# Performance work log

Hardware: AMD Instinct MI355X
Metric: run time of the kernel (lower is better)

Reference implementation:

```python
import jax, jax.numpy as jnp
import numpy as np

HEAD_NUM = 16
EMBED_DIM = 1024
HIDDEN_DIM = 1024
HEAD_DIM = HIDDEN_DIM // HEAD_NUM


def setup_inputs() -> dict:
    key = jax.random.key(0)
    ks = jax.random.split(key, 7)
    B, S = 2, 2048
    X = jax.random.normal(ks[0], (B, S, EMBED_DIM), dtype=jnp.float32)
    sc = 1.0 / np.sqrt(EMBED_DIM)
    Wq = jax.random.normal(ks[1], (EMBED_DIM, HIDDEN_DIM), dtype=jnp.float32) * sc
    Wk = jax.random.normal(ks[2], (EMBED_DIM, HIDDEN_DIM), dtype=jnp.float32) * sc
    Wv = jax.random.normal(ks[3], (EMBED_DIM, HIDDEN_DIM), dtype=jnp.float32) * sc
    bq = jax.random.normal(ks[4], (HIDDEN_DIM,), dtype=jnp.float32) * 0.01
    bk = jax.random.normal(ks[5], (HIDDEN_DIM,), dtype=jnp.float32) * 0.01
    bv = jax.random.normal(ks[6], (HIDDEN_DIM,), dtype=jnp.float32) * 0.01
    return {"X": X, "Wq": Wq, "bq": bq, "Wk": Wk, "bk": bk, "Wv": Wv, "bv": bv}


def reference(X, Wq, bq, Wk, bk, Wv, bv):
    B, S, _ = X.shape
    # projections -> [B, H, S, D]
    def split_heads(t):
        return t.reshape(B, S, HEAD_NUM, HEAD_DIM).transpose(0, 2, 1, 3)
    Q = split_heads(X @ Wq + bq)
    K = split_heads(X @ Wk + bk)  # computed but unused, faithful to source bug
    V = split_heads(X @ Wv + bv)
    # NOTE: source computes Q @ V^T (bug), reproduced faithfully
    scores = jnp.einsum('bhqd,bhkd->bhqk', Q, V) / np.sqrt(HEAD_DIM)
    attn = jax.nn.softmax(scores, axis=-1)  # dropout is identity in eval
    out = jnp.einsum('bhqk,bhkd->bhqd', attn, V)
    return out.transpose(0, 2, 1, 3).reshape(B, S, HIDDEN_DIM)
```

## Files before the change

### kernel.cpp

```cpp
#include <hip/hip_runtime.h>
#include <math.h>


constexpr int BATCH = 2;
constexpr int SEQ   = 2048;
constexpr int EMB   = 1024;
constexpr int NHEAD = 16;
constexpr int HDIM  = 64;
constexpr int HID   = 1024;

typedef __attribute__((ext_vector_type(8))) _Float16 half8;
typedef __attribute__((ext_vector_type(4))) float    f32x4;

#define MFMA16(a, b, c) __builtin_amdgcn_mfma_f32_16x16x32_f16((a), (b), (c), 0, 0, 0)

constexpr int LDT = 80;

#define QK_SCALE 0.18033688011112042f
#define LOG2_THR 11.0f

__device__ __forceinline__ _Float16 f2h(float f) { return (_Float16)f; }

__global__ __launch_bounds__(256) void conv_wt_kernel(
    const float* __restrict__ W0, _Float16* __restrict__ WT0,
    const float* __restrict__ W1, _Float16* __restrict__ WT1)
{
    const float*  W  = blockIdx.z ? W1  : W0;
    _Float16*     WT = blockIdx.z ? WT1 : WT0;
    __shared__ _Float16 T[64 * 68];
    const int tid = threadIdx.x;
    const int n0 = blockIdx.x * 64;
    const int k0 = blockIdx.y * 64;

    #pragma unroll
    for (int i = 0; i < 4; ++i) {
        const int u = tid + i * 256;
        const int r = u >> 4;
        const int c4 = (u & 15) << 2;
        const float4 v = *(const float4*)&W[(size_t)(k0 + r) * HID + n0 + c4];
        T[r * 68 + c4 + 0] = f2h(v.x);
        T[r * 68 + c4 + 1] = f2h(v.y);
        T[r * 68 + c4 + 2] = f2h(v.z);
        T[r * 68 + c4 + 3] = f2h(v.w);
    }
    __syncthreads();

    union Pack { uint4 q; _Float16 e[8]; };
    #pragma unroll
    for (int i = 0; i < 2; ++i) {
        const int u = tid + i * 256;
        const int n = u >> 3;
        const int kc = (u & 7) << 3;
        Pack p;
        #pragma unroll
        for (int j = 0; j < 8; ++j) p.e[j] = T[(kc + j) * 68 + n];
        *(uint4*)&WT[(size_t)(n0 + n) * EMB + k0 + kc] = p.q;
    }
}

__global__ __launch_bounds__(256) void proj_kernel(
    const float* __restrict__ X, const _Float16* __restrict__ WTq,
    const _Float16* __restrict__ WTv, const float* __restrict__ bq,
    const float* __restrict__ bv, _Float16* __restrict__ Qo,
    _Float16* __restrict__ Vo, _Float16* __restrict__ VTo)
{
    __shared__ __align__(16) _Float16 Xs[64 * LDT];
    __shared__ __align__(16) _Float16 Wqs[64 * LDT];
    __shared__ __align__(16) _Float16 Wvs[64 * LDT];

    const int tid  = threadIdx.x;
    const int lane = tid & 63;
    const int w    = tid >> 6;
    const int l15  = lane & 15;
    const int l4   = lane >> 4;
    const int wg   = blockIdx.x;
    const int nid  = (wg & 7) * 128 + (wg >> 3);
    const int mblk = nid >> 4;
    const int h    = nid & 15;
    const int m0   = mblk * 64;
    const int n0   = h * HDIM;

    f32x4 aq[4], av[4];
    #pragma unroll
    for (int nt = 0; nt < 4; ++nt) {
        aq[nt] = f32x4{0.f, 0.f, 0.f, 0.f};
        av[nt] = f32x4{0.f, 0.f, 0.f, 0.f};
    }

    for (int k0 = 0; k0 < EMB; k0 += 64) {
        #pragma unroll
        for (int i = 0; i < 4; ++i) {
            const int u = tid + i * 256;
            const int r = u >> 4;
            const int c4 = (u & 15) << 2;
            const float4 v = *(const float4*)&X[(size_t)(m0 + r) * EMB + k0 + c4];
            Xs[r * LDT + c4 + 0] = f2h(v.x);
            Xs[r * LDT + c4 + 1] = f2h(v.y);
            Xs[r * LDT + c4 + 2] = f2h(v.z);
            Xs[r * LDT + c4 + 3] = f2h(v.w);
        }
        #pragma unroll
        for (int i = 0; i < 2; ++i) {
            const int u = tid + i * 256;
            const int r = u >> 3;
            const int c8 = (u & 7) << 3;
            *(uint4*)&Wqs[r * LDT + c8] =
                *(const uint4*)&WTq[(size_t)(n0 + r) * EMB + k0 + c8];
            *(uint4*)&Wvs[r * LDT + c8] =
                *(const uint4*)&WTv[(size_t)(n0 + r) * EMB + k0 + c8];
        }
        __syncthreads();

        __builtin_amdgcn_s_setprio(1);
        #pragma unroll
        for (int kd = 0; kd < 2; ++kd) {
            const int ko = kd * 32 + l4 * 8;
            half8 xa = *(const half8*)&Xs[(w * 16 + l15) * LDT + ko];
            #pragma unroll
            for (int nt = 0; nt < 4; ++nt) {
                half8 wq = *(const half8*)&Wqs[(nt * 16 + l15) * LDT + ko];
                half8 wv = *(const half8*)&Wvs[(nt * 16 + l15) * LDT + ko];
                aq[nt] = MFMA16(xa, wq, aq[nt]);
                av[nt] = MFMA16(xa, wv, av[nt]);
            }
        }
        __builtin_amdgcn_s_setprio(0);
        __syncthreads();
    }

    constexpr int LV = 65;
    _Float16* Vlds = Xs;
    const int bb = m0 >> 11;
    const int sb = m0 & (SEQ - 1);
    const int bh = bb * NHEAD + h;

    #pragma unroll
    for (int nt = 0; nt < 4; ++nt) {
        const int d = nt * 16 + l15;
        const float bqv = bq[n0 + d];
        const float bvv = bv[n0 + d];
        #pragma unroll
        for (int r = 0; r < 4; ++r) {
            const int sl = w * 16 + l4 * 4 + r;
            const int s  = sb + sl;
            const _Float16 vh = f2h(av[nt][r] + bvv);
            Qo[((size_t)bh * SEQ + s) * HDIM + d] =
                f2h((aq[nt][r] + bqv) * QK_SCALE);
            Vo[((size_t)bh * SEQ + s) * HDIM + d] = vh;
            Vlds[sl * LV + d] = vh;
        }
    }
    __syncthreads();

    union PK { uint4 q; _Float16 e[8]; };
    #pragma unroll
    for (int i = 0; i < 2; ++i) {
        const int c  = tid + i * 256;
        const int d  = c >> 3;
        const int sc = (c & 7) << 3;
        PK p;
        #pragma unroll
        for (int j = 0; j < 8; ++j) p.e[j] = Vlds[(sc + j) * LV + d];
        *(uint4*)&VTo[((size_t)bh * HDIM + d) * SEQ + sb + sc] = p.q;
    }
}

__global__ __launch_bounds__(256) void attn_kernel(
    const _Float16* __restrict__ Qw, const _Float16* __restrict__ Vw,
    const _Float16* __restrict__ VTw, float* __restrict__ out)
{
    __shared__ __align__(16) _Float16 PQs[64 * LDT];
    __shared__ __align__(16) _Float16 Vs[64 * LDT];
    __shared__ __align__(16) _Float16 VTs[80 * LDT];

    const int tid  = threadIdx.x;
    const int lane = tid & 63;
    const int w    = tid >> 6;
    const int l15  = lane & 15;
    const int l4   = lane >> 4;
    const int wg = blockIdx.x;
    const int nw = (wg & 7) * 128 + (wg >> 3);
    const int bh = nw >> 5;
    const int qb = nw & 31;
    const int b  = bh >> 4;
    const int h  = bh & (NHEAD - 1);
    const int s0 = qb * 64;

    const _Float16* Qp  = Qw  + (size_t)bh * SEQ * HDIM;
    const _Float16* Vp  = Vw  + (size_t)bh * SEQ * HDIM;
    const _Float16* VTp = VTw + (size_t)bh * HDIM * SEQ;

    auto stageV = [&](int t) {
        const int u0 = tid,       r0 = u0 >> 3, c0 = (u0 & 7) << 3;
        const int u1 = tid + 256, r1 = u1 >> 3, c1 = (u1 & 7) << 3;
        uint4 a0 = *(const uint4*)&Vp [(size_t)(t * 64 + r0) * HDIM + c0];
        uint4 a1 = *(const uint4*)&Vp [(size_t)(t * 64 + r1) * HDIM + c1];
        uint4 b0 = *(const uint4*)&VTp[(size_t)r0 * SEQ + t * 64 + c0];
        uint4 b1 = *(const uint4*)&VTp[(size_t)r1 * SEQ + t * 64 + c1];
        *(uint4*)&Vs [r0 * LDT + c0] = a0;
        *(uint4*)&Vs [r1 * LDT + c1] = a1;
        *(uint4*)&VTs[r0 * LDT + c0] = b0;
        *(uint4*)&VTs[r1 * LDT + c1] = b1;
    };

    #pragma unroll
    for (int i = 0; i < 2; ++i) {
        const int u = tid + i * 256, r = u >> 3, c8 = (u & 7) << 3;
        *(uint4*)&PQs[r * LDT + c8] =
            *(const uint4*)&Qp[(size_t)(s0 + r) * HDIM + c8];
    }
    #pragma unroll
    for (int i = 0; i < 5; ++i) {
        const int idx = tid + i * 256;
        if (idx < 16 * LDT)
            VTs[64 * LDT + idx] = (idx < LDT) ? (_Float16)1.0f : (_Float16)0.0f;
    }
    stageV(0);
    __syncthreads();

    const half8 qa0 = *(const half8*)&PQs[(w * 16 + l15) * LDT + l4 * 8];
    const half8 qa1 = *(const half8*)&PQs[(w * 16 + l15) * LDT + 32 + l4 * 8];

    f32x4 acc_o[5];
    #pragma unroll
    for (int dt = 0; dt < 5; ++dt) acc_o[dt] = f32x4{0.f, 0.f, 0.f, 0.f};
    float m_i[4] = {-INFINITY, -INFINITY, -INFINITY, -INFINITY};

    const int chi  = l15 >> 3;
    const int hl   = l15 & 7;
    const int rkey = l15 & 7;

    for (int t = 0; t < SEQ / 64; ++t) {
        f32x4 acc_s[4];
        #pragma unroll
        for (int nt = 0; nt < 4; ++nt) acc_s[nt] = f32x4{0.f, 0.f, 0.f, 0.f};
        __builtin_amdgcn_s_setprio(1);
        #pragma unroll
        for (int nt = 0; nt < 4; ++nt) {
            half8 vb0 = *(const half8*)&Vs[(nt * 16 + l15) * LDT + l4 * 8];
            half8 vb1 = *(const half8*)&Vs[(nt * 16 + l15) * LDT + 32 + l4 * 8];
            acc_s[nt] = MFMA16(qa0, vb0, acc_s[nt]);
            acc_s[nt] = MFMA16(qa1, vb1, acc_s[nt]);
        }
        __builtin_amdgcn_s_setprio(0);

        float mloc[4];
        int needf = 0;
        #pragma unroll
        for (int r = 0; r < 4; ++r) {
            float ml = fmaxf(fmaxf(acc_s[0][r], acc_s[1][r]),
                             fmaxf(acc_s[2][r], acc_s[3][r]));
            #pragma unroll
            for (int off = 1; off < 16; off <<= 1)
                ml = fmaxf(ml, __shfl_xor(ml, off));
            mloc[r] = ml;
            needf |= (ml > m_i[r] + LOG2_THR) ? 1 : 0;
        }
        if (__any(needf)) {
            #pragma unroll
            for (int r = 0; r < 4; ++r) {
                const float mnew = fmaxf(m_i[r], mloc[r]);
                const float corr = __builtin_amdgcn_exp2f(m_i[r] - mnew);
                m_i[r] = mnew;
                #pragma unroll
                for (int dt = 0; dt < 5; ++dt) acc_o[dt][r] *= corr;
            }
        }
        #pragma unroll
        for (int r = 0; r < 4; ++r) {
            const float p0 = __builtin_amdgcn_exp2f(acc_s[0][r] - m_i[r]);
            const float p1 = __builtin_amdgcn_exp2f(acc_s[1][r] - m_i[r]);
            const float p2 = __builtin_amdgcn_exp2f(acc_s[2][r] - m_i[r]);
            const float p3 = __builtin_amdgcn_exp2f(acc_s[3][r] - m_i[r]);
            const int key = (l4 * 4 + r) & 7;
            _Float16* pr = &PQs[(w * 16 + l4 * 4 + r) * LDT];
            pr[(((0 + chi) ^ key) << 3) + hl] = f2h(p0);
            pr[(((2 + chi) ^ key) << 3) + hl] = f2h(p1);
            pr[(((4 + chi) ^ key) << 3) + hl] = f2h(p2);
            pr[(((6 + chi) ^ key) << 3) + hl] = f2h(p3);
        }

        const _Float16* prd = &PQs[(w * 16 + l15) * LDT];
        half8 pa0 = *(const half8*)&prd[((l4 ^ rkey) << 3)];
        half8 pa1 = *(const half8*)&prd[(((4 + l4) ^ rkey) << 3)];
        __builtin_amdgcn_s_setprio(1);
        #pragma unroll
        for (int dt = 0; dt < 5; ++dt) {
            half8 vt0 = *(const half8*)&VTs[(dt * 16 + l15) * LDT + l4 * 8];
            half8 vt1 = *(const half8*)&VTs[(dt * 16 + l15) * LDT + 32 + l4 * 8];
            acc_o[dt] = MFMA16(pa0, vt0, acc_o[dt]);
            acc_o[dt] = MFMA16(pa1, vt1, acc_o[dt]);
        }
        __builtin_amdgcn_s_setprio(0);

        __syncthreads();
        if (t + 1 < SEQ / 64) {
            stageV(t + 1);
            __syncthreads();
        }
    }

    #pragma unroll
    for (int r = 0; r < 4; ++r) {
        const float ls  = __shfl(acc_o[4][r], (lane & 48));
        const float inv = 1.f / ls;
        const int s = s0 + w * 16 + l4 * 4 + r;
        float* op = &out[((size_t)(b * SEQ + s)) * HID + h * HDIM + l15];
        op[ 0] = acc_o[0][r] * inv;
        op[16] = acc_o[1][r] * inv;
        op[32] = acc_o[2][r] * inv;
        op[48] = acc_o[3][r] * inv;
    }
}

extern "C" void kernel_launch(void* const* d_in, const int* in_sizes, int n_in,
                              void* d_out, int out_size, void* d_ws, size_t ws_size,
                              hipStream_t stream) {
    (void)in_sizes; (void)n_in; (void)out_size; (void)ws_size;
    const float* X  = (const float*)d_in[0];
    const float* Wq = (const float*)d_in[1];
    const float* bq = (const float*)d_in[2];
    const float* Wv = (const float*)d_in[5];
    const float* bv = (const float*)d_in[6];
    float* outp = (float*)d_out;

    char* ws = (char*)d_ws;
    _Float16* WTq = (_Float16*)(ws);
    _Float16* WTv = (_Float16*)(ws + (2u  << 20));
    _Float16* Qb  = (_Float16*)(ws + (4u  << 20));
    _Float16* Vb  = (_Float16*)(ws + (12u << 20));
    _Float16* VTb = (_Float16*)(ws + (20u << 20));

    conv_wt_kernel<<<dim3(16, 16, 2), 256, 0, stream>>>(Wq, WTq, Wv, WTv);
    proj_kernel<<<1024, 256, 0, stream>>>(X, WTq, WTv, bq, bv, Qb, Vb, VTb);
    attn_kernel<<<1024, 256, 0, stream>>>(Qb, Vb, VTb, outp);
}
```

Baseline: 229.0 us.

## Pre-convert X to fp16, enlarge projection tiles, double-buffer with direct LDS loads

Adds a pass that converts X to swizzled fp16 ahead of time and writes the transposed weights with a matching XOR swizzle. The projection kernel now computes a 256-row by one-head tile per block, with 4x4 MFMA tiles per wave. Its operands are double-buffered through global_load_lds so the next K slice loads while the current one is multiplied. This is meant to cut redundant weight reads, remove the fp32 conversion from the inner loop, and avoid LDS bank conflicts. In exchange the grid drops to 256 blocks at one block per CU, uses much more LDS and registers, and adds an extra kernel launch plus a round trip of X through memory.

```diff
diff --git a/kernel.cpp b/kernel.cpp
--- a/kernel.cpp
+++ b/kernel.cpp
@@ -20,6 +20,30 @@
 #define LOG2_THR 11.0f
 
 __device__ __forceinline__ _Float16 f2h(float f) { return (_Float16)f; }
+
+__device__ __forceinline__ void gl16(const _Float16* g, _Float16* l) {
+    __builtin_amdgcn_global_load_lds(
+        (const __attribute__((address_space(1))) void*)g,
+        (__attribute__((address_space(3))) void*)l, 16, 0, 0);
+}
+
+__global__ __launch_bounds__(256) void conv_x_kernel(
+    const float* __restrict__ X, _Float16* __restrict__ Xz)
+{
+    const int idx = blockIdx.x * 256 + threadIdx.x;
+    const int m  = idx >> 7;
+    const int cg = idx & 127;
+    const int g8 = cg >> 3;
+    const int c  = cg & 7;
+    const int cs = c ^ (m & 7);
+    const float* s = &X[(size_t)m * EMB + g8 * 64 + cs * 8];
+    const float4 a = *(const float4*)s;
+    const float4 b = *(const float4*)(s + 4);
+    union { uint4 q; _Float16 e[8]; } p;
+    p.e[0] = f2h(a.x); p.e[1] = f2h(a.y); p.e[2] = f2h(a.z); p.e[3] = f2h(a.w);
+    p.e[4] = f2h(b.x); p.e[5] = f2h(b.y); p.e[6] = f2h(b.z); p.e[7] = f2h(b.w);
+    *(uint4*)&Xz[(size_t)m * EMB + g8 * 64 + c * 8] = p.q;
+}
 
 __global__ __launch_bounds__(256) void conv_wt_kernel(
     const float* __restrict__ W0, _Float16* __restrict__ WT0,
@@ -50,82 +74,101 @@
     for (int i = 0; i < 2; ++i) {
         const int u = tid + i * 256;
         const int n = u >> 3;
-        const int kc = (u & 7) << 3;
+        const int cdst = u & 7;
+        const int ks = ((cdst ^ (n & 7)) << 3);
         Pack p;
         #pragma unroll
-        for (int j = 0; j < 8; ++j) p.e[j] = T[(kc + j) * 68 + n];
-        *(uint4*)&WT[(size_t)(n0 + n) * EMB + k0 + kc] = p.q;
-    }
-}
-
-__global__ __launch_bounds__(256) void proj_kernel(
-    const float* __restrict__ X, const _Float16* __restrict__ WTq,
+        for (int j = 0; j < 8; ++j) p.e[j] = T[(ks + j) * 68 + n];
+        *(uint4*)&WT[(size_t)(n0 + n) * EMB + k0 + (cdst << 3)] = p.q;
+    }
+}
+
+__global__ __launch_bounds__(256, 1) void proj_kernel(
+    const _Float16* __restrict__ Xz, const _Float16* __restrict__ WTq,
     const _Float16* __restrict__ WTv, const float* __restrict__ bq,
     const float* __restrict__ bv, _Float16* __restrict__ Qo,
     _Float16* __restrict__ Vo, _Float16* __restrict__ VTo)
 {
-    __shared__ __align__(16) _Float16 Xs[64 * LDT];
-    __shared__ __align__(16) _Float16 Wqs[64 * LDT];
-    __shared__ __align__(16) _Float16 Wvs[64 * LDT];
+    __shared__ __align__(16) _Float16 Xs[2 * 256 * 64];
+    __shared__ __align__(16) _Float16 Wqs[2 * 64 * 64];
+    __shared__ __align__(16) _Float16 Wvs[2 * 64 * 64];
 
     const int tid  = threadIdx.x;
     const int lane = tid & 63;
     const int w    = tid >> 6;
     const int l15  = lane & 15;
     const int l4   = lane >> 4;
-    const int wg   = blockIdx.x;
-    const int nid  = (wg & 7) * 128 + (wg >> 3);
-    const int mblk = nid >> 4;
-    const int h    = nid & 15;
-    const int m0   = mblk * 64;
-    const int n0   = h * HDIM;
-
-    f32x4 aq[4], av[4];
-    #pragma unroll
-    for (int nt = 0; nt < 4; ++nt) {
-        aq[nt] = f32x4{0.f, 0.f, 0.f, 0.f};
-        av[nt] = f32x4{0.f, 0.f, 0.f, 0.f};
-    }
-
-    for (int k0 = 0; k0 < EMB; k0 += 64) {
-        #pragma unroll
-        for (int i = 0; i < 4; ++i) {
-            const int u = tid + i * 256;
-            const int r = u >> 4;
-            const int c4 = (u & 15) << 2;
-            const float4 v = *(const float4*)&X[(size_t)(m0 + r) * EMB + k0 + c4];
-            Xs[r * LDT + c4 + 0] = f2h(v.x);
-            Xs[r * LDT + c4 + 1] = f2h(v.y);
-            Xs[r * LDT + c4 + 2] = f2h(v.z);
-            Xs[r * LDT + c4 + 3] = f2h(v.w);
-        }
+    const int wg  = blockIdx.x;
+    const int nid = (wg & 7) * 32 + (wg >> 3);
+    const int mg  = nid >> 4;
+    const int h   = nid & 15;
+    const int m0  = mg * 256;
+    const int n0  = h * HDIM;
+
+    const int lr = lane >> 3;
+    const int lc = (lane & 7) << 3;
+
+    f32x4 aq[4][4], av[4][4];
+    #pragma unroll
+    for (int mt = 0; mt < 4; ++mt)
+        #pragma unroll
+        for (int nt = 0; nt < 4; ++nt) {
+            aq[mt][nt] = f32x4{0.f, 0.f, 0.f, 0.f};
+            av[mt][nt] = f32x4{0.f, 0.f, 0.f, 0.f};
+        }
+
+    auto stage = [&](int k0, int b) {
+        _Float16* xb = &Xs[b * (256 * 64)];
+        const _Float16* gx = Xz + (size_t)(m0 + w * 64) * EMB + k0;
+        #pragma unroll
+        for (int i = 0; i < 8; ++i)
+            gl16(&gx[(size_t)(i * 8 + lr) * EMB + lc], &xb[(w * 64 + i * 8) * 64]);
+        _Float16* qb = &Wqs[b * (64 * 64)];
+        _Float16* vb = &Wvs[b * (64 * 64)];
+        const _Float16* gq = WTq + (size_t)(n0 + w * 16) * EMB + k0;
+        const _Float16* gv = WTv + (size_t)(n0 + w * 16) * EMB + k0;
         #pragma unroll
         for (int i = 0; i < 2; ++i) {
-            const int u = tid + i * 256;
-            const int r = u >> 3;
-            const int c8 = (u & 7) << 3;
-            *(uint4*)&Wqs[r * LDT + c8] =
-                *(const uint4*)&WTq[(size_t)(n0 + r) * EMB + k0 + c8];
-            *(uint4*)&Wvs[r * LDT + c8] =
-                *(const uint4*)&WTv[(size_t)(n0 + r) * EMB + k0 + c8];
-        }
-        __syncthreads();
-
+            gl16(&gq[(size_t)(i * 8 + lr) * EMB + lc], &qb[(w * 16 + i * 8) * 64]);
+            gl16(&gv[(size_t)(i * 8 + lr) * EMB + lc], &vb[(w * 16 + i * 8) * 64]);
+        }
+    };
+
+    stage(0, 0);
+    __syncthreads();
+
+    int buf = 0;
+    const int key = l15 & 7;
+    for (int t = 0; t < 16; ++t) {
+        if (t < 15) stage((t + 1) * 64, buf ^ 1);
+
+        const _Float16* xb = &Xs[buf * (256 * 64)];
+        const _Float16* qb = &Wqs[buf * (64 * 64)];
+        const _Float16* vb = &Wvs[buf * (64 * 64)];
         __builtin_amdgcn_s_setprio(1);
         #pragma unroll
         for (int kd = 0; kd < 2; ++kd) {
-            const int ko = kd * 32 + l4 * 8;
-            half8 xa = *(const half8*)&Xs[(w * 16 + l15) * LDT + ko];
+            const int ch = ((kd * 4 + l4) ^ key) << 3;
+            half8 xa[4], wq[4], wv[4];
+            #pragma unroll
+            for (int mt = 0; mt < 4; ++mt)
+                xa[mt] = *(const half8*)&xb[(w * 64 + mt * 16 + l15) * 64 + ch];
             #pragma unroll
             for (int nt = 0; nt < 4; ++nt) {
-                half8 wq = *(const half8*)&Wqs[(nt * 16 + l15) * LDT + ko];
-                half8 wv = *(const half8*)&Wvs[(nt * 16 + l15) * LDT + ko];
-                aq[nt] = MFMA16(xa, wq, aq[nt]);
-                av[nt] = MFMA16(xa, wv, av[nt]);
+                wq[nt] = *(const half8*)&qb[(nt * 16 + l15) * 64 + ch];
+                wv[nt] = *(const half8*)&vb[(nt * 16 + l15) * 64 + ch];
             }
+            #pragma unroll
+            for (int mt = 0; mt < 4; ++mt)
+                #pragma unroll
+                for (int nt = 0; nt < 4; ++nt) {
+                    aq[mt][nt] = MFMA16(xa[mt], wq[nt], aq[mt][nt]);
+                    av[mt][nt] = MFMA16(xa[mt], wv[nt], av[mt][nt]);
+                }
         }
         __builtin_amdgcn_s_setprio(0);
         __syncthreads();
+        buf ^= 1;
     }
 
     constexpr int LV = 65;
@@ -140,24 +183,26 @@
         const float bqv = bq[n0 + d];
         const float bvv = bv[n0 + d];
         #pragma unroll
-        for (int r = 0; r < 4; ++r) {
-            const int sl = w * 16 + l4 * 4 + r;
-            const int s  = sb + sl;
-            const _Float16 vh = f2h(av[nt][r] + bvv);
-            Qo[((size_t)bh * SEQ + s) * HDIM + d] =
-                f2h((aq[nt][r] + bqv) * QK_SCALE);
-            Vo[((size_t)bh * SEQ + s) * HDIM + d] = vh;
-            Vlds[sl * LV + d] = vh;
-        }
+        for (int mt = 0; mt < 4; ++mt)
+            #pragma unroll
+            for (int r = 0; r < 4; ++r) {
+                const int sl = w * 64 + mt * 16 + l4 * 4 + r;
+                const int s  = sb + sl;
+                const _Float16 vh = f2h(av[mt][nt][r] + bvv);
+                Qo[((size_t)bh * SEQ + s) * HDIM + d] =
+                    f2h((aq[mt][nt][r] + bqv) * QK_SCALE);
+                Vo[((size_t)bh * SEQ + s) * HDIM + d] = vh;
+                Vlds[sl * LV + d] = vh;
+            }
     }
     __syncthreads();
 
     union PK { uint4 q; _Float16 e[8]; };
     #pragma unroll
-    for (int i = 0; i < 2; ++i) {
-        const int c  = tid + i * 256;
-        const int d  = c >> 3;
-        const int sc = (c & 7) << 3;
+    for (int i = 0; i < 8; ++i) {
+        const int cix = tid + i * 256;
+        const int d  = cix >> 5;
+        const int sc = (cix & 31) << 3;
         PK p;
         #pragma unroll
         for (int j = 0; j < 8; ++j) p.e[j] = Vlds[(sc + j) * LV + d];
@@ -325,13 +370,15 @@
     float* outp = (float*)d_out;
 
     char* ws = (char*)d_ws;
-    _Float16* WTq = (_Float16*)(ws);
-    _Float16* WTv = (_Float16*)(ws + (2u  << 20));
-    _Float16* Qb  = (_Float16*)(ws + (4u  << 20));
-    _Float16* Vb  = (_Float16*)(ws + (12u << 20));
-    _Float16* VTb = (_Float16*)(ws + (20u << 20));
-
+    _Float16* Xz  = (_Float16*)(ws);
+    _Float16* WTq = (_Float16*)(ws + (8u  << 20));
+    _Float16* WTv = (_Float16*)(ws + (10u << 20));
+    _Float16* Qb  = (_Float16*)(ws + (12u << 20));
+    _Float16* Vb  = (_Float16*)(ws + (20u << 20));
+    _Float16* VTb = (_Float16*)(ws + (28u << 20));
+
+    conv_x_kernel<<<2048, 256, 0, stream>>>(X, Xz);
     conv_wt_kernel<<<dim3(16, 16, 2), 256, 0, stream>>>(Wq, WTq, Wv, WTv);
-    proj_kernel<<<1024, 256, 0, stream>>>(X, WTq, WTv, bq, bv, Qb, Vb, VTb);
+    proj_kernel<<<256, 256, 0, stream>>>(Xz, WTq, WTv, bq, bv, Qb, Vb, VTb);
     attn_kernel<<<1024, 256, 0, stream>>>(Qb, Vb, VTb, outp);
 }
```

New measurement: 202.0 us. -11.8%, faster.
